# Kernel optimization log

Hardware: AMD Instinct MI355X
Metric: run time of the kernel (lower is better)

Reference implementation:

```python
import jax, jax.numpy as jnp
import numpy as np

HEADS = 4
DIM_HEAD = 32
DIM = 64
NUM_MEM = 4


def _rmsnorm(t, g, dim):
    # F.normalize(x, dim=1) * g * sqrt(dim)  (eps=1e-12 like torch)
    n = jnp.sqrt(jnp.sum(t * t, axis=1, keepdims=True))
    return t / jnp.maximum(n, 1e-12) * g * (dim ** 0.5)


def setup_inputs() -> dict:
    key = jax.random.key(0)
    ks = jax.random.split(key, 7)
    b, c, H, W, D = 2, DIM, 48, 48, 48
    hidden = HEADS * DIM_HEAD
    x = jax.random.normal(ks[0], (b, c, H, W, D), dtype=jnp.float32)
    g_in = jnp.ones((1, c, 1, 1, 1), dtype=jnp.float32)
    w_qkv = jax.random.normal(ks[1], (hidden * 3, c), dtype=jnp.float32) * 0.02  # 1x1 conv3d
    mem_kv = jax.random.normal(ks[2], (2, HEADS, DIM_HEAD, NUM_MEM), dtype=jnp.float32)
    w_out = jax.random.normal(ks[3], (c, hidden), dtype=jnp.float32) * 0.02
    b_out = jnp.zeros((c,), dtype=jnp.float32)
    g_out = jnp.ones((1, c, 1, 1, 1), dtype=jnp.float32)
    return {"x": x, "g_in": g_in, "w_qkv": w_qkv, "mem_kv": mem_kv,
            "w_out": w_out, "b_out": b_out, "g_out": g_out}


def reference(x, g_in, w_qkv, mem_kv, w_out, b_out, g_out):
    b, c, H, W, D = x.shape
    n = H * W * D
    scale = DIM_HEAD ** -0.5
    xn = _rmsnorm(x, g_in, c)
    # 1x1 conv3d == channel matmul
    qkv = jnp.einsum('oc,bcxyz->boxyz', w_qkv, xn)
    q, k, v = jnp.split(qkv, 3, axis=1)
    to_heads = lambda t: t.reshape(b, HEADS, DIM_HEAD, n)
    q, k, v = map(to_heads, (q, k, v))
    mk = jnp.broadcast_to(mem_kv[0], (b, HEADS, DIM_HEAD, NUM_MEM))
    mv = jnp.broadcast_to(mem_kv[1], (b, HEADS, DIM_HEAD, NUM_MEM))
    k = jnp.concatenate([mk, k], axis=-1)
    v = jnp.concatenate([mv, v], axis=-1)
    q = jax.nn.softmax(q, axis=-2) * scale  # softmax over head dim
    k = jax.nn.softmax(k, axis=-1)          # softmax over sequence dim
    context = jnp.einsum('bhdn,bhen->bhde', k, v)   # [b,h,d,e]
    out = jnp.einsum('bhde,bhdn->bhen', context, q)  # [b,h,e,n]
    out = out.reshape(b, HEADS * DIM_HEAD, H, W, D)
    out = jnp.einsum('oc,bcxyz->boxyz', w_out, out) + b_out[None, :, None, None, None]
    return _rmsnorm(out, g_out, c)
```

## Files before the change

### kernel.cpp

```cpp
#include <hip/hip_runtime.h>
#include <math.h>

#define NPOS 110592

typedef float f32x4 __attribute__((ext_vector_type(4)));
typedef short bf16x8 __attribute__((ext_vector_type(8)));
typedef unsigned u32;
typedef u32 u32x2 __attribute__((ext_vector_type(2)));
typedef u32 u32x4 __attribute__((ext_vector_type(4)));

#define MFMA __builtin_amdgcn_mfma_f32_16x16x32_bf16

__device__ __forceinline__ short f2bf(float f) {
    u32 u = __builtin_bit_cast(u32, f);
    u += 0x7fffu + ((u >> 16) & 1u);
    return (short)(u >> 16);
}
__device__ __forceinline__ u32 pack2(float a, float b) {
    return (u32)(unsigned short)f2bf(a) | ((u32)(unsigned short)f2bf(b) << 16);
}

union FragU { u32 w[4]; bf16x8 v; };
__device__ __forceinline__ bf16x8 padfrag(u32 a, u32 b) {
    FragU f; f.w[0] = a; f.w[1] = b; f.w[2] = 0u; f.w[3] = 0u; return f.v;
}

__global__ __launch_bounds__(256) void la_prep(const float* __restrict__ wqkv,
                                               const float* __restrict__ g_in,
                                               short* __restrict__ wqkv_bf)
{
    int i = blockIdx.x * 256 + threadIdx.x;
    if (i < 24576) wqkv_bf[i] = f2bf(wqkv[i] * g_in[i & 63]);
}

__global__ __launch_bounds__(256, 3) void la_p01(
    const float* __restrict__ x, const short* __restrict__ wkv,
    short* __restrict__ xnT, float* __restrict__ partials)
{
    __shared__ __align__(16) char smem[34816];
    char* xnz = smem;
    float (*lctx)[2][32][33] = (float (*)[2][32][33])smem;
    float (*lz)[2][32]       = (float (*)[2][32])(smem + 33792);

    const int tid = threadIdx.x, lane = tid & 63, wid = tid >> 6;
    const int g = lane >> 4, m = lane & 15;
    const int blk = blockIdx.x;
    const int batch = blk / 432;
    const int pb = (blk % 432) * 256;

    const float* base = x + (size_t)batch * 64 * NPOS + pb + tid;
    float xv[64]; float ss = 0.f;
#pragma unroll
    for (int c = 0; c < 64; ++c) { float t = base[(size_t)c * NPOS]; xv[c] = t; ss += t * t; }
    float rn = 8.0f / fmaxf(sqrtf(ss), 1e-12f);

    char* row = xnz + tid * 128;
#pragma unroll
    for (int ch = 0; ch < 8; ++ch) {
        u32x4 w;
        w.x = pack2(xv[ch*8+0] * rn, xv[ch*8+1] * rn);
        w.y = pack2(xv[ch*8+2] * rn, xv[ch*8+3] * rn);
        w.z = pack2(xv[ch*8+4] * rn, xv[ch*8+5] * rn);
        w.w = pack2(xv[ch*8+6] * rn, xv[ch*8+7] * rn);
        *(u32x4*)(row + ((ch ^ (tid & 7)) << 4)) = w;
    }
    __syncthreads();

    const int cg = wid >> 1, hbase = (wid & 1) * 2;

    bf16x8 wkA[2][2][2], wvA[2][2][2];
#pragma unroll
    for (int hh = 0; hh < 2; ++hh) {
#pragma unroll
        for (int dt = 0; dt < 2; ++dt) {
            const short* wr = wkv + (size_t)(128 + (hbase + hh) * 32 + dt * 16 + m) * 64 + g * 8;
            wkA[hh][dt][0] = *(const bf16x8*)wr;
            wkA[hh][dt][1] = *(const bf16x8*)(wr + 32);
        }
#pragma unroll
        for (int et = 0; et < 2; ++et) {
            const short* wr = wkv + (size_t)(256 + (hbase + hh) * 32 + et * 16 + m) * 64 + g * 8;
            wvA[hh][et][0] = *(const bf16x8*)wr;
            wvA[hh][et][1] = *(const bf16x8*)(wr + 32);
        }
    }

    f32x4 acc[2][2][2];
#pragma unroll
    for (int hh = 0; hh < 2; ++hh)
#pragma unroll
        for (int dt = 0; dt < 2; ++dt)
#pragma unroll
            for (int et = 0; et < 2; ++et) acc[hh][dt][et] = (f32x4){0.f, 0.f, 0.f, 0.f};
    float zacc[2][2] = {{0.f, 0.f}, {0.f, 0.f}};

#pragma unroll 1
    for (int ic = 0; ic < 4; ++ic) {
        bf16x8 af[2][2];
#pragma unroll
        for (int mt = 0; mt < 2; ++mt)
#pragma unroll
            for (int kf = 0; kf < 2; ++kf) {
                int rowi = cg * 128 + ic * 32 + mt * 16 + m;
                af[mt][kf] = *(const bf16x8*)(xnz + rowi * 128 + (((kf*4+g) ^ (rowi & 7)) << 4));
            }
#pragma unroll
        for (int hh = 0; hh < 2; ++hh) {
            u32 ek[2][2][2], vv[2][2][2];
#pragma unroll
            for (int dt = 0; dt < 2; ++dt) {
#pragma unroll
                for (int mt = 0; mt < 2; ++mt) {
                    f32x4 a = {0.f, 0.f, 0.f, 0.f};
                    a = MFMA(af[mt][0], wkA[hh][dt][0], a, 0, 0, 0);
                    a = MFMA(af[mt][1], wkA[hh][dt][1], a, 0, 0, 0);
                    float e0 = __expf(a[0]), e1 = __expf(a[1]);
                    float e2 = __expf(a[2]), e3 = __expf(a[3]);
                    zacc[hh][dt] += (e0 + e1) + (e2 + e3);
                    ek[dt][mt][0] = pack2(e0, e1);
                    ek[dt][mt][1] = pack2(e2, e3);
                }
            }
#pragma unroll
            for (int et = 0; et < 2; ++et) {
#pragma unroll
                for (int mt = 0; mt < 2; ++mt) {
                    f32x4 a = {0.f, 0.f, 0.f, 0.f};
                    a = MFMA(af[mt][0], wvA[hh][et][0], a, 0, 0, 0);
                    a = MFMA(af[mt][1], wvA[hh][et][1], a, 0, 0, 0);
                    vv[et][mt][0] = pack2(a[0], a[1]);
                    vv[et][mt][1] = pack2(a[2], a[3]);
                }
            }
#pragma unroll
            for (int dt = 0; dt < 2; ++dt)
#pragma unroll
                for (int et = 0; et < 2; ++et)
#pragma unroll
                    for (int mt = 0; mt < 2; ++mt)
                        acc[hh][dt][et] = MFMA(padfrag(ek[dt][mt][0], ek[dt][mt][1]),
                                               padfrag(vv[et][mt][0], vv[et][mt][1]),
                                               acc[hh][dt][et], 0, 0, 0);
        }
    }

    char* dst = (char*)xnT + ((size_t)batch * NPOS + pb) * 128;
#pragma unroll
    for (int i = 0; i < 8; ++i) {
        int u = i * 256 + tid;
        int r = u >> 3, cl = u & 7;
        u32x4 w = *(const u32x4*)(xnz + r * 128 + ((cl ^ (r & 7)) << 4));
        *(u32x4*)(dst + (size_t)u * 16) = w;
    }

    __syncthreads();
#pragma unroll
    for (int hh = 0; hh < 2; ++hh) {
#pragma unroll
        for (int dt = 0; dt < 2; ++dt) {
#pragma unroll
            for (int et = 0; et < 2; ++et)
#pragma unroll
                for (int r4 = 0; r4 < 4; ++r4)
                    lctx[wid][hh][dt * 16 + g * 4 + r4][et * 16 + m] = acc[hh][dt][et][r4];
            float z = zacc[hh][dt];
            z += __shfl_xor(z, 16);
            z += __shfl_xor(z, 32);
            if (g == 0) lz[wid][hh][dt * 16 + m] = z;
        }
    }
    __syncthreads();

    float* P = partials + (size_t)blk * 4224;
    for (int i = tid; i < 4096; i += 256) {
        int h = i >> 10, de = i & 1023, d = de >> 5, e = de & 31;
        int w0 = h >> 1, hh2 = h & 1;
        P[i] = lctx[w0][hh2][d][e] + lctx[w0 + 2][hh2][d][e];
    }
    if (tid < 128) {
        int h = tid >> 5, d = tid & 31;
        P[4096 + tid] = lz[h >> 1][h & 1][d] + lz[(h >> 1) + 2][h & 1][d];
    }
}

__global__ __launch_bounds__(256) void la_ctxt_a(const float* __restrict__ partials,
                                                 float* __restrict__ part2)
{
    int t = blockIdx.x * 256 + threadIdx.x;
    int b = t / 67584;
    int rem = t % 67584;
    int grp = rem / 4224;
    int i = rem % 4224;
    const float* P = partials + ((size_t)(b * 432 + grp * 27)) * 4224 + i;
    float s = 0.f;
#pragma unroll 3
    for (int j = 0; j < 27; ++j) s += P[(size_t)j * 4224];
    part2[((size_t)(b * 16 + grp)) * 4224 + i] = s;
}

__global__ __launch_bounds__(256) void la_ctxt_b(const float* __restrict__ part2,
                                                 const float* __restrict__ mem_kv,
                                                 const float* __restrict__ wout_f,
                                                 short* __restrict__ W2bf)
{
    __shared__ float ctxN[32][33];
    const int tid = threadIdx.x;
    const int b = blockIdx.x >> 2, h = blockIdx.x & 3;
    const float* P = part2 + (size_t)b * 16 * 4224;
#pragma unroll
    for (int u = 0; u < 4; ++u) {
        int de = tid * 4 + u;
        int d = de >> 5, e = de & 31;
        float S = 0.f, Z = 0.f;
#pragma unroll 4
        for (int grp = 0; grp < 16; ++grp) {
            S += P[(size_t)grp * 4224 + h * 1024 + de];
            Z += P[(size_t)grp * 4224 + 4096 + h * 32 + d];
        }
        const float* mk = mem_kv + (h * 32 + d) * 4;
        const float* mv = mem_kv + 512 + (h * 32 + e) * 4;
#pragma unroll
        for (int mm = 0; mm < 4; ++mm) {
            float ekv = __expf(mk[mm]);
            S += ekv * mv[mm];
            Z += ekv;
        }
        ctxN[d][e] = S / Z;
    }
    __syncthreads();
#pragma unroll
    for (int u = 0; u < 8; ++u) {
        int idx = u * 256 + tid;
        int c = idx >> 5, d = idx & 31;
        const float* wr = wout_f + c * 128 + h * 32;
        float s = 0.f;
#pragma unroll
        for (int e = 0; e < 32; ++e) s += wr[e] * ctxN[d][e];
        W2bf[(size_t)(b * 64 + c) * 128 + h * 32 + d] = f2bf(s);
    }
}

__global__ __launch_bounds__(256, 2) void la_pass2(
    const short* __restrict__ xnT, const short* __restrict__ wq,
    const short* __restrict__ W2, const float* __restrict__ b_out,
    const float* __restrict__ g_out, float* __restrict__ out)
{
    const int tid = threadIdx.x, lane = tid & 63, wid = tid >> 6;
    const int g = lane >> 4, m = lane & 15;
    const int blk = blockIdx.x;
    const int batch = blk / 432;
    const int task = (blk % 432) * 4 + wid;
    const int posbase = task * 64;

    const short* xp = xnT + ((size_t)batch * NPOS + posbase) * 64;
    bf16x8 af[4][2];
#pragma unroll
    for (int mt = 0; mt < 4; ++mt)
#pragma unroll
        for (int kf = 0; kf < 2; ++kf)
            af[mt][kf] = *(const bf16x8*)(xp + (mt * 16 + m) * 64 + kf * 32 + g * 8);

    f32x4 oacc[4][4];
#pragma unroll
    for (int ct = 0; ct < 4; ++ct)
#pragma unroll
        for (int mt = 0; mt < 4; ++mt) oacc[ct][mt] = (f32x4){0.f, 0.f, 0.f, 0.f};

    const float scale = 0.17677669529663687f;
    const short* w2b = W2 + (size_t)batch * 8192;

#pragma unroll 1
    for (int h = 0; h < 4; ++h) {
        f32x4 aa[2][4];
#pragma unroll
        for (int dt = 0; dt < 2; ++dt) {
            const short* wr = wq + (size_t)(h * 32 + dt * 16 + m) * 64 + g * 8;
            bf16x8 a0 = *(const bf16x8*)wr;
            bf16x8 a1 = *(const bf16x8*)(wr + 32);
#pragma unroll
            for (int mt = 0; mt < 4; ++mt) {
                f32x4 a = {0.f, 0.f, 0.f, 0.f};
                a = MFMA(a0, af[mt][0], a, 0, 0, 0);
                a = MFMA(a1, af[mt][1], a, 0, 0, 0);
                aa[dt][mt][0] = __expf(a[0]);
                aa[dt][mt][1] = __expf(a[1]);
                aa[dt][mt][2] = __expf(a[2]);
                aa[dt][mt][3] = __expf(a[3]);
            }
        }
        float inv[4];
#pragma unroll
        for (int mt = 0; mt < 4; ++mt) {
            float dn = (aa[0][mt][0] + aa[0][mt][1]) + (aa[0][mt][2] + aa[0][mt][3])
                     + (aa[1][mt][0] + aa[1][mt][1]) + (aa[1][mt][2] + aa[1][mt][3]);
            dn += __shfl_xor(dn, 16);
            dn += __shfl_xor(dn, 32);
            inv[mt] = scale / dn;
        }
        u32 eqn[2][4][2];
#pragma unroll
        for (int dt = 0; dt < 2; ++dt)
#pragma unroll
            for (int mt = 0; mt < 4; ++mt) {
                eqn[dt][mt][0] = pack2(aa[dt][mt][0] * inv[mt], aa[dt][mt][1] * inv[mt]);
                eqn[dt][mt][1] = pack2(aa[dt][mt][2] * inv[mt], aa[dt][mt][3] * inv[mt]);
            }
#pragma unroll
        for (int ct = 0; ct < 4; ++ct)
#pragma unroll
            for (int dt = 0; dt < 2; ++dt) {
                u32x2 wv = *(const u32x2*)(w2b + (ct * 16 + m) * 128 + h * 32 + dt * 16 + g * 4);
                bf16x8 wfr = padfrag(wv.x, wv.y);
#pragma unroll
                for (int mt = 0; mt < 4; ++mt)
                    oacc[ct][mt] = MFMA(wfr, padfrag(eqn[dt][mt][0], eqn[dt][mt][1]),
                                        oacc[ct][mt], 0, 0, 0);
            }
    }

    float bo[4][4], go[4][4];
#pragma unroll
    for (int ct = 0; ct < 4; ++ct)
#pragma unroll
        for (int r = 0; r < 4; ++r) {
            int c = ct * 16 + g * 4 + r;
            bo[ct][r] = b_out[c];
            go[ct][r] = g_out[c];
        }
    float* ob = out + (size_t)batch * 64 * NPOS;
#pragma unroll
    for (int mt = 0; mt < 4; ++mt) {
        float vv[4][4]; float s2 = 0.f;
#pragma unroll
        for (int ct = 0; ct < 4; ++ct)
#pragma unroll
            for (int r = 0; r < 4; ++r) {
                float v = oacc[ct][mt][r] + bo[ct][r];
                vv[ct][r] = v;
                s2 += v * v;
            }
        s2 += __shfl_xor(s2, 16);
        s2 += __shfl_xor(s2, 32);
        float rn2 = 8.0f / fmaxf(sqrtf(s2), 1e-12f);
        int pn = posbase + mt * 16 + m;
#pragma unroll
        for (int ct = 0; ct < 4; ++ct)
#pragma unroll
            for (int r = 0; r < 4; ++r)
                ob[(size_t)(ct * 16 + g * 4 + r) * NPOS + pn] = vv[ct][r] * rn2 * go[ct][r];
    }
}

extern "C" void kernel_launch(void* const* d_in, const int* in_sizes, int n_in,
                              void* d_out, int out_size, void* d_ws, size_t ws_size,
                              hipStream_t stream) {
    const float* x      = (const float*)d_in[0];
    const float* g_in   = (const float*)d_in[1];
    const float* w_qkv  = (const float*)d_in[2];
    const float* mem_kv = (const float*)d_in[3];
    const float* w_out  = (const float*)d_in[4];
    const float* b_out  = (const float*)d_in[5];
    const float* g_out  = (const float*)d_in[6];
    float* out = (float*)d_out;

    char* ws = (char*)d_ws;
    short* xnT     = (short*)(ws);
    float* part2   = (float*)(ws + 28311552);
    short* wqkv_bf = (short*)(ws + 28852224);
    short* W2bf    = (short*)(ws + 28901376);

    float* partials = (float*)d_out;

    la_prep<<<96, 256, 0, stream>>>(w_qkv, g_in, wqkv_bf);
    la_p01<<<864, 256, 0, stream>>>(x, wqkv_bf, xnT, partials);
    la_ctxt_a<<<528, 256, 0, stream>>>(partials, part2);
    la_ctxt_b<<<8, 256, 0, stream>>>(part2, mem_kv, w_out, W2bf);
    la_pass2<<<864, 256, 0, stream>>>(xnT, wqkv_bf, W2bf, b_out, g_out, out);
}
```

Before: 98.02 us.

## Fuse linear-attention passes into one cooperative persistent kernel with grid syncs

```diff
diff --git a/kernel.cpp b/kernel.cpp
--- a/kernel.cpp
+++ b/kernel.cpp
@@ -1,5 +1,8 @@
 #include <hip/hip_runtime.h>
+#include <hip/hip_cooperative_groups.h>
 #include <math.h>
+
+namespace cg = cooperative_groups;
 
 #define NPOS 110592
 
@@ -31,6 +34,297 @@
 {
     int i = blockIdx.x * 256 + threadIdx.x;
     if (i < 24576) wqkv_bf[i] = f2bf(wqkv[i] * g_in[i & 63]);
+}
+
+__global__ __launch_bounds__(256, 4) void la_fused(
+    const float* __restrict__ x, const short* __restrict__ wqkv,
+    const float* __restrict__ mem_kv, const float* __restrict__ wout_f,
+    const float* __restrict__ b_out, const float* __restrict__ g_out,
+    float* __restrict__ partials, float* __restrict__ ctxG,
+    short* __restrict__ W2bf, float* __restrict__ out)
+{
+    __shared__ __align__(16) char xnz[32768];
+    __shared__ float lctx[32][33];
+    __shared__ float lz[32];
+
+    const int tid = threadIdx.x, lane = tid & 63, wid = tid >> 6;
+    const int g = lane >> 4, m = lane & 15;
+    const int blk = blockIdx.x;
+    const int batch = blk / 432;
+    const int pb = (blk % 432) * 256;
+
+    {
+        const float* base = x + (size_t)batch * 64 * NPOS + pb + tid;
+        float xv[64]; float ss = 0.f;
+#pragma unroll
+        for (int c = 0; c < 64; ++c) { float t = base[(size_t)c * NPOS]; xv[c] = t; ss += t * t; }
+        float rn = 8.0f / fmaxf(sqrtf(ss), 1e-12f);
+        char* row = xnz + tid * 128;
+#pragma unroll
+        for (int ch = 0; ch < 8; ++ch) {
+            u32x4 w;
+            w.x = pack2(xv[ch*8+0] * rn, xv[ch*8+1] * rn);
+            w.y = pack2(xv[ch*8+2] * rn, xv[ch*8+3] * rn);
+            w.z = pack2(xv[ch*8+4] * rn, xv[ch*8+5] * rn);
+            w.w = pack2(xv[ch*8+6] * rn, xv[ch*8+7] * rn);
+            *(u32x4*)(row + ((ch ^ (tid & 7)) << 4)) = w;
+        }
+    }
+    __syncthreads();
+
+    const int cgrp = wid >> 1, hbase = (wid & 1) * 2;
+    f32x4 acc[2][2][2];
+#pragma unroll
+    for (int hh = 0; hh < 2; ++hh)
+#pragma unroll
+        for (int dt = 0; dt < 2; ++dt)
+#pragma unroll
+            for (int et = 0; et < 2; ++et) acc[hh][dt][et] = (f32x4){0.f, 0.f, 0.f, 0.f};
+    float zacc[2][2] = {{0.f, 0.f}, {0.f, 0.f}};
+
+#pragma unroll 1
+    for (int ic = 0; ic < 4; ++ic) {
+        bf16x8 af[2][2];
+#pragma unroll
+        for (int mt = 0; mt < 2; ++mt)
+#pragma unroll
+            for (int kf = 0; kf < 2; ++kf) {
+                int rowi = cgrp * 128 + ic * 32 + mt * 16 + m;
+                af[mt][kf] = *(const bf16x8*)(xnz + rowi * 128 + (((kf*4+g) ^ (rowi & 7)) << 4));
+            }
+#pragma unroll
+        for (int hh = 0; hh < 2; ++hh) {
+            const int h = hbase + hh;
+            u32 ek[2][2][2], vv[2][2][2];
+#pragma unroll
+            for (int dt = 0; dt < 2; ++dt) {
+                const short* wr = wqkv + (size_t)(128 + h * 32 + dt * 16 + m) * 64 + g * 8;
+                bf16x8 w0 = *(const bf16x8*)wr;
+                bf16x8 w1 = *(const bf16x8*)(wr + 32);
+#pragma unroll
+                for (int mt = 0; mt < 2; ++mt) {
+                    f32x4 a = {0.f, 0.f, 0.f, 0.f};
+                    a = MFMA(af[mt][0], w0, a, 0, 0, 0);
+                    a = MFMA(af[mt][1], w1, a, 0, 0, 0);
+                    float e0 = __expf(a[0]), e1 = __expf(a[1]);
+                    float e2 = __expf(a[2]), e3 = __expf(a[3]);
+                    zacc[hh][dt] += (e0 + e1) + (e2 + e3);
+                    ek[dt][mt][0] = pack2(e0, e1);
+                    ek[dt][mt][1] = pack2(e2, e3);
+                }
+            }
+#pragma unroll
+            for (int et = 0; et < 2; ++et) {
+                const short* wr = wqkv + (size_t)(256 + h * 32 + et * 16 + m) * 64 + g * 8;
+                bf16x8 w0 = *(const bf16x8*)wr;
+                bf16x8 w1 = *(const bf16x8*)(wr + 32);
+#pragma unroll
+                for (int mt = 0; mt < 2; ++mt) {
+                    f32x4 a = {0.f, 0.f, 0.f, 0.f};
+                    a = MFMA(af[mt][0], w0, a, 0, 0, 0);
+                    a = MFMA(af[mt][1], w1, a, 0, 0, 0);
+                    vv[et][mt][0] = pack2(a[0], a[1]);
+                    vv[et][mt][1] = pack2(a[2], a[3]);
+                }
+            }
+#pragma unroll
+            for (int dt = 0; dt < 2; ++dt)
+#pragma unroll
+                for (int et = 0; et < 2; ++et)
+#pragma unroll
+                    for (int mt = 0; mt < 2; ++mt)
+                        acc[hh][dt][et] = MFMA(padfrag(ek[dt][mt][0], ek[dt][mt][1]),
+                                               padfrag(vv[et][mt][0], vv[et][mt][1]),
+                                               acc[hh][dt][et], 0, 0, 0);
+        }
+    }
+
+    float ctxsum[4][4];
+#pragma unroll
+    for (int H = 0; H < 4; ++H)
+#pragma unroll
+        for (int k = 0; k < 4; ++k) ctxsum[H][k] = 0.f;
+    float zsum = 0.f;
+
+#pragma unroll
+    for (int r = 0; r < 8; ++r) {
+        const int w = r >> 1, hh = r & 1;
+        const int H = (w & 1) * 2 + hh;
+        if (wid == w) {
+#pragma unroll
+            for (int dt = 0; dt < 2; ++dt) {
+#pragma unroll
+                for (int et = 0; et < 2; ++et)
+#pragma unroll
+                    for (int r4 = 0; r4 < 4; ++r4)
+                        lctx[dt * 16 + g * 4 + r4][et * 16 + m] = acc[hh][dt][et][r4];
+                float z = zacc[hh][dt];
+                z += __shfl_xor(z, 16);
+                z += __shfl_xor(z, 32);
+                if (g == 0) lz[dt * 16 + m] = z;
+            }
+        }
+        __syncthreads();
+#pragma unroll
+        for (int k = 0; k < 4; ++k) {
+            int cell = tid * 4 + k;
+            ctxsum[H][k] += lctx[cell >> 5][cell & 31];
+        }
+        if ((tid >> 5) == H) zsum += lz[tid & 31];
+        __syncthreads();
+    }
+    {
+        float* P = partials + (size_t)blk * 4224;
+#pragma unroll
+        for (int H = 0; H < 4; ++H) {
+            f32x4 v;
+            v[0] = ctxsum[H][0]; v[1] = ctxsum[H][1];
+            v[2] = ctxsum[H][2]; v[3] = ctxsum[H][3];
+            *(f32x4*)(P + H * 1024 + tid * 4) = v;
+        }
+        if (tid < 128) P[4096 + tid] = zsum;
+    }
+
+    cg::this_grid().sync();
+
+    if (blk < 132) {
+        int t = blk * 256 + tid;
+        int q = t / 8448;
+        int u = t % 8448;
+        int b = u / 4224, i = u % 4224;
+        const float* Q = partials + ((size_t)(b * 432 + q * 108)) * 4224 + i;
+        float s = 0.f;
+#pragma unroll 8
+        for (int j = 0; j < 108; ++j) s += Q[(size_t)j * 4224];
+        atomicAdd(&ctxG[b * 4224 + i], s);
+    }
+    cg::this_grid().sync();
+
+    if (blk < 8) {
+        float (*ctxN)[33] = lctx;
+        const int b = blk >> 2, h = blk & 3;
+#pragma unroll
+        for (int u = 0; u < 4; ++u) {
+            int de = tid * 4 + u;
+            int d = de >> 5, e = de & 31;
+            float S = ctxG[b * 4224 + h * 1024 + de];
+            float Z = ctxG[b * 4224 + 4096 + h * 32 + d];
+            const float* mk = mem_kv + (h * 32 + d) * 4;
+            const float* mv = mem_kv + 512 + (h * 32 + e) * 4;
+#pragma unroll
+            for (int mm = 0; mm < 4; ++mm) {
+                float ekv = __expf(mk[mm]);
+                S += ekv * mv[mm];
+                Z += ekv;
+            }
+            ctxN[d][e] = S / Z;
+        }
+        __syncthreads();
+#pragma unroll
+        for (int u = 0; u < 8; ++u) {
+            int idx = u * 256 + tid;
+            int c = idx >> 5, d = idx & 31;
+            const float* wr = wout_f + c * 128 + h * 32;
+            float s = 0.f;
+#pragma unroll
+            for (int e = 0; e < 32; ++e) s += wr[e] * ctxN[d][e];
+            W2bf[(size_t)(b * 64 + c) * 128 + h * 32 + d] = f2bf(s);
+        }
+    }
+    cg::this_grid().sync();
+
+    const short* w2b = W2bf + (size_t)batch * 8192;
+    const float scale = 0.17677669529663687f;
+    float* ob = out + (size_t)batch * 64 * NPOS;
+
+#pragma unroll 1
+    for (int half = 0; half < 2; ++half) {
+        bf16x8 af[2][2];
+#pragma unroll
+        for (int mt = 0; mt < 2; ++mt)
+#pragma unroll
+            for (int kf = 0; kf < 2; ++kf) {
+                int rowi = wid * 64 + half * 32 + mt * 16 + m;
+                af[mt][kf] = *(const bf16x8*)(xnz + rowi * 128 + (((kf*4+g) ^ (rowi & 7)) << 4));
+            }
+        f32x4 oacc[4][2];
+#pragma unroll
+        for (int ct = 0; ct < 4; ++ct)
+#pragma unroll
+            for (int mt = 0; mt < 2; ++mt) oacc[ct][mt] = (f32x4){0.f, 0.f, 0.f, 0.f};
+
+#pragma unroll 1
+        for (int h = 0; h < 4; ++h) {
+            f32x4 aa[2][2];
+#pragma unroll
+            for (int dt = 0; dt < 2; ++dt) {
+                const short* wr = wqkv + (size_t)(h * 32 + dt * 16 + m) * 64 + g * 8;
+                bf16x8 a0 = *(const bf16x8*)wr;
+                bf16x8 a1 = *(const bf16x8*)(wr + 32);
+#pragma unroll
+                for (int mt = 0; mt < 2; ++mt) {
+                    f32x4 a = {0.f, 0.f, 0.f, 0.f};
+                    a = MFMA(a0, af[mt][0], a, 0, 0, 0);
+                    a = MFMA(a1, af[mt][1], a, 0, 0, 0);
+                    aa[dt][mt][0] = __expf(a[0]);
+                    aa[dt][mt][1] = __expf(a[1]);
+                    aa[dt][mt][2] = __expf(a[2]);
+                    aa[dt][mt][3] = __expf(a[3]);
+                }
+            }
+            float inv[2];
+#pragma unroll
+            for (int mt = 0; mt < 2; ++mt) {
+                float dn = (aa[0][mt][0] + aa[0][mt][1]) + (aa[0][mt][2] + aa[0][mt][3])
+                         + (aa[1][mt][0] + aa[1][mt][1]) + (aa[1][mt][2] + aa[1][mt][3]);
+                dn += __shfl_xor(dn, 16);
+                dn += __shfl_xor(dn, 32);
+                inv[mt] = scale / dn;
+            }
+            u32 eqn[2][2][2];
+#pragma unroll
+            for (int dt = 0; dt < 2; ++dt)
+#pragma unroll
+                for (int mt = 0; mt < 2; ++mt) {
+                    eqn[dt][mt][0] = pack2(aa[dt][mt][0] * inv[mt], aa[dt][mt][1] * inv[mt]);
+                    eqn[dt][mt][1] = pack2(aa[dt][mt][2] * inv[mt], aa[dt][mt][3] * inv[mt]);
+                }
+#pragma unroll
+            for (int ct = 0; ct < 4; ++ct)
+#pragma unroll
+                for (int dt = 0; dt < 2; ++dt) {
+                    u32x2 wv = *(const u32x2*)(w2b + (ct * 16 + m) * 128 + h * 32 + dt * 16 + g * 4);
+                    bf16x8 wfr = padfrag(wv.x, wv.y);
+#pragma unroll
+                    for (int mt = 0; mt < 2; ++mt)
+                        oacc[ct][mt] = MFMA(wfr, padfrag(eqn[dt][mt][0], eqn[dt][mt][1]),
+                                            oacc[ct][mt], 0, 0, 0);
+                }
+        }
+
+#pragma unroll
+        for (int mt = 0; mt < 2; ++mt) {
+            float vv[4][4]; float s2 = 0.f;
+#pragma unroll
+            for (int ct = 0; ct < 4; ++ct)
+#pragma unroll
+                for (int r = 0; r < 4; ++r) {
+                    float v = oacc[ct][mt][r] + b_out[ct * 16 + g * 4 + r];
+                    vv[ct][r] = v;
+                    s2 += v * v;
+                }
+            s2 += __shfl_xor(s2, 16);
+            s2 += __shfl_xor(s2, 32);
+            float rn2 = 8.0f / fmaxf(sqrtf(s2), 1e-12f);
+            int pn = pb + wid * 64 + half * 32 + mt * 16 + m;
+#pragma unroll
+            for (int ct = 0; ct < 4; ++ct)
+#pragma unroll
+                for (int r = 0; r < 4; ++r)
+                    ob[(size_t)(ct * 16 + g * 4 + r) * NPOS + pn] =
+                        vv[ct][r] * rn2 * g_out[ct * 16 + g * 4 + r];
+        }
+    }
 }
 
 __global__ __launch_bounds__(256, 3) void la_p01(
@@ -53,7 +347,6 @@
 #pragma unroll
     for (int c = 0; c < 64; ++c) { float t = base[(size_t)c * NPOS]; xv[c] = t; ss += t * t; }
     float rn = 8.0f / fmaxf(sqrtf(ss), 1e-12f);
-
     char* row = xnz + tid * 128;
 #pragma unroll
     for (int ch = 0; ch < 8; ++ch) {
@@ -66,8 +359,7 @@
     }
     __syncthreads();
 
-    const int cg = wid >> 1, hbase = (wid & 1) * 2;
-
+    const int cgrp = wid >> 1, hbase = (wid & 1) * 2;
     bf16x8 wkA[2][2][2], wvA[2][2][2];
 #pragma unroll
     for (int hh = 0; hh < 2; ++hh) {
@@ -84,7 +376,6 @@
             wvA[hh][et][1] = *(const bf16x8*)(wr + 32);
         }
     }
-
     f32x4 acc[2][2][2];
 #pragma unroll
     for (int hh = 0; hh < 2; ++hh)
@@ -101,14 +392,14 @@
         for (int mt = 0; mt < 2; ++mt)
 #pragma unroll
             for (int kf = 0; kf < 2; ++kf) {
-                int rowi = cg * 128 + ic * 32 + mt * 16 + m;
+                int rowi = cgrp * 128 + ic * 32 + mt * 16 + m;
                 af[mt][kf] = *(const bf16x8*)(xnz + rowi * 128 + (((kf*4+g) ^ (rowi & 7)) << 4));
             }
 #pragma unroll
         for (int hh = 0; hh < 2; ++hh) {
             u32 ek[2][2][2], vv[2][2][2];
 #pragma unroll
-            for (int dt = 0; dt < 2; ++dt) {
+            for (int dt = 0; dt < 2; ++dt)
 #pragma unroll
                 for (int mt = 0; mt < 2; ++mt) {
                     f32x4 a = {0.f, 0.f, 0.f, 0.f};
@@ -120,9 +411,8 @@
                     ek[dt][mt][0] = pack2(e0, e1);
                     ek[dt][mt][1] = pack2(e2, e3);
                 }
-            }
-#pragma unroll
-            for (int et = 0; et < 2; ++et) {
+#pragma unroll
+            for (int et = 0; et < 2; ++et)
 #pragma unroll
                 for (int mt = 0; mt < 2; ++mt) {
                     f32x4 a = {0.f, 0.f, 0.f, 0.f};
@@ -131,7 +421,6 @@
                     vv[et][mt][0] = pack2(a[0], a[1]);
                     vv[et][mt][1] = pack2(a[2], a[3]);
                 }
-            }
 #pragma unroll
             for (int dt = 0; dt < 2; ++dt)
 #pragma unroll
@@ -155,7 +444,7 @@
 
     __syncthreads();
 #pragma unroll
-    for (int hh = 0; hh < 2; ++hh) {
+    for (int hh = 0; hh < 2; ++hh)
 #pragma unroll
         for (int dt = 0; dt < 2; ++dt) {
 #pragma unroll
@@ -168,7 +457,6 @@
             z += __shfl_xor(z, 32);
             if (g == 0) lz[wid][hh][dt * 16 + m] = z;
         }
-    }
     __syncthreads();
 
     float* P = partials + (size_t)blk * 4224;
@@ -364,16 +652,38 @@
     float* out = (float*)d_out;
 
     char* ws = (char*)d_ws;
-    short* xnT     = (short*)(ws);
-    float* part2   = (float*)(ws + 28311552);
-    short* wqkv_bf = (short*)(ws + 28852224);
-    short* W2bf    = (short*)(ws + 28901376);
-
-    float* partials = (float*)d_out;
-
-    la_prep<<<96, 256, 0, stream>>>(w_qkv, g_in, wqkv_bf);
-    la_p01<<<864, 256, 0, stream>>>(x, wqkv_bf, xnT, partials);
-    la_ctxt_a<<<528, 256, 0, stream>>>(partials, part2);
-    la_ctxt_b<<<8, 256, 0, stream>>>(part2, mem_kv, w_out, W2bf);
-    la_pass2<<<864, 256, 0, stream>>>(xnT, wqkv_bf, W2bf, b_out, g_out, out);
-}
+    float* partials = (float*)ws;
+    float* ctxG     = (float*)(ws + 14598144);
+    short* wqkv_bf  = (short*)(ws + 14631936);
+    short* W2bf     = (short*)(ws + 14681088);
+
+    int nb = 0;
+    hipError_t qe = hipOccupancyMaxActiveBlocksPerMultiprocessor(
+        &nb, reinterpret_cast<const void*>(la_fused), 256, 0);
+    if (qe == hipSuccess && nb >= 4) {
+        la_prep<<<96, 256, 0, stream>>>(w_qkv, g_in, wqkv_bf);
+        hipMemsetAsync(ctxG, 0, 33792, stream);
+        const float* xa = x; const short* wa = wqkv_bf;
+        const float* ma = mem_kv; const float* wo = w_out;
+        const float* ba = b_out; const float* ga = g_out;
+        float* pa = partials; float* ca = ctxG; short* w2a = W2bf; float* oa = out;
+        void* args[] = {(void*)&xa, (void*)&wa, (void*)&ma, (void*)&wo, (void*)&ba,
+                        (void*)&ga, (void*)&pa, (void*)&ca, (void*)&w2a, (void*)&oa};
+        hipError_t e = hipLaunchCooperativeKernel(
+            reinterpret_cast<const void*>(la_fused), dim3(864), dim3(256), args, 0, stream);
+        if (e == hipSuccess) return;
+        (void)hipGetLastError();
+    }
+
+    short* xnT      = (short*)ws;
+    float* part2    = (float*)(ws + 28311552);
+    short* wqkv_bf2 = (short*)(ws + 28852224);
+    short* W2bf2    = (short*)(ws + 28901376);
+    float* partialsF = (float*)d_out;
+
+    la_prep<<<96, 256, 0, stream>>>(w_qkv, g_in, wqkv_bf2);
+    la_p01<<<864, 256, 0, stream>>>(x, wqkv_bf2, xnT, partialsF);
+    la_ctxt_a<<<528, 256, 0, stream>>>(partialsF, part2);
+    la_ctxt_b<<<8, 256, 0, stream>>>(part2, mem_kv, w_out, W2bf2);
+    la_pass2<<<864, 256, 0, stream>>>(xnT, wqkv_bf2, W2bf2, b_out, g_out, out);
+}
```

New measurement: 97.56 us. No clear change (-0.5%).

## Halve la_p01 tile to 128 positions, split channel loads across thread pairs

Applied to the files above, without the earlier changes.

```diff
diff --git a/kernel.cpp b/kernel.cpp
--- a/kernel.cpp
+++ b/kernel.cpp
@@ -33,36 +33,39 @@
     if (i < 24576) wqkv_bf[i] = f2bf(wqkv[i] * g_in[i & 63]);
 }
 
-__global__ __launch_bounds__(256, 3) void la_p01(
+__global__ __launch_bounds__(256, 6) void la_p01(
     const float* __restrict__ x, const short* __restrict__ wkv,
     short* __restrict__ xnT, float* __restrict__ partials)
 {
-    __shared__ __align__(16) char smem[34816];
+    __shared__ __align__(16) char smem[17920];
     char* xnz = smem;
     float (*lctx)[2][32][33] = (float (*)[2][32][33])smem;
-    float (*lz)[2][32]       = (float (*)[2][32])(smem + 33792);
+    float (*lz)[2][32]       = (float (*)[2][32])(smem + 16896);
 
     const int tid = threadIdx.x, lane = tid & 63, wid = tid >> 6;
     const int g = lane >> 4, m = lane & 15;
     const int blk = blockIdx.x;
-    const int batch = blk / 432;
-    const int pb = (blk % 432) * 256;
-
-    const float* base = x + (size_t)batch * 64 * NPOS + pb + tid;
-    float xv[64]; float ss = 0.f;
-#pragma unroll
-    for (int c = 0; c < 64; ++c) { float t = base[(size_t)c * NPOS]; xv[c] = t; ss += t * t; }
-    float rn = 8.0f / fmaxf(sqrtf(ss), 1e-12f);
-
-    char* row = xnz + tid * 128;
-#pragma unroll
-    for (int ch = 0; ch < 8; ++ch) {
-        u32x4 w;
-        w.x = pack2(xv[ch*8+0] * rn, xv[ch*8+1] * rn);
-        w.y = pack2(xv[ch*8+2] * rn, xv[ch*8+3] * rn);
-        w.z = pack2(xv[ch*8+4] * rn, xv[ch*8+5] * rn);
-        w.w = pack2(xv[ch*8+6] * rn, xv[ch*8+7] * rn);
-        *(u32x4*)(row + ((ch ^ (tid & 7)) << 4)) = w;
+    const int batch = blk / 864;
+    const int pb = (blk % 864) * 128;
+
+    {
+        const int p = tid >> 1, chb = (tid & 1) * 32;
+        const float* base = x + ((size_t)batch * 64 + chb) * NPOS + pb + p;
+        float xv[32]; float ss = 0.f;
+#pragma unroll
+        for (int c = 0; c < 32; ++c) { float t = base[(size_t)c * NPOS]; xv[c] = t; ss += t * t; }
+        ss += __shfl_xor(ss, 1);
+        float rn = 8.0f / fmaxf(sqrtf(ss), 1e-12f);
+#pragma unroll
+        for (int q = 0; q < 4; ++q) {
+            u32x4 w;
+            w.x = pack2(xv[q*8+0] * rn, xv[q*8+1] * rn);
+            w.y = pack2(xv[q*8+2] * rn, xv[q*8+3] * rn);
+            w.z = pack2(xv[q*8+4] * rn, xv[q*8+5] * rn);
+            w.w = pack2(xv[q*8+6] * rn, xv[q*8+7] * rn);
+            int ch = (tid & 1) * 4 + q;
+            *(u32x4*)(xnz + p * 128 + ((ch ^ (p & 7)) << 4)) = w;
+        }
     }
     __syncthreads();
 
@@ -95,13 +98,13 @@
     float zacc[2][2] = {{0.f, 0.f}, {0.f, 0.f}};
 
 #pragma unroll 1
-    for (int ic = 0; ic < 4; ++ic) {
+    for (int ic = 0; ic < 2; ++ic) {
         bf16x8 af[2][2];
 #pragma unroll
         for (int mt = 0; mt < 2; ++mt)
 #pragma unroll
             for (int kf = 0; kf < 2; ++kf) {
-                int rowi = cg * 128 + ic * 32 + mt * 16 + m;
+                int rowi = cg * 64 + ic * 32 + mt * 16 + m;
                 af[mt][kf] = *(const bf16x8*)(xnz + rowi * 128 + (((kf*4+g) ^ (rowi & 7)) << 4));
             }
 #pragma unroll
@@ -146,7 +149,7 @@
 
     char* dst = (char*)xnT + ((size_t)batch * NPOS + pb) * 128;
 #pragma unroll
-    for (int i = 0; i < 8; ++i) {
+    for (int i = 0; i < 4; ++i) {
         int u = i * 256 + tid;
         int r = u >> 3, cl = u & 7;
         u32x4 w = *(const u32x4*)(xnz + r * 128 + ((cl ^ (r & 7)) << 4));
@@ -154,32 +157,50 @@
     }
 
     __syncthreads();
-#pragma unroll
-    for (int hh = 0; hh < 2; ++hh) {
-#pragma unroll
-        for (int dt = 0; dt < 2; ++dt) {
-#pragma unroll
-            for (int et = 0; et < 2; ++et)
-#pragma unroll
-                for (int r4 = 0; r4 < 4; ++r4)
-                    lctx[wid][hh][dt * 16 + g * 4 + r4][et * 16 + m] = acc[hh][dt][et][r4];
-            float z = zacc[hh][dt];
-            z += __shfl_xor(z, 16);
-            z += __shfl_xor(z, 32);
-            if (g == 0) lz[wid][hh][dt * 16 + m] = z;
-        }
+    const int hp = wid & 1;
+    if (wid < 2) {
+#pragma unroll
+        for (int hh = 0; hh < 2; ++hh)
+#pragma unroll
+            for (int dt = 0; dt < 2; ++dt) {
+#pragma unroll
+                for (int et = 0; et < 2; ++et)
+#pragma unroll
+                    for (int r4 = 0; r4 < 4; ++r4)
+                        lctx[hp][hh][dt * 16 + g * 4 + r4][et * 16 + m] = acc[hh][dt][et][r4];
+                float z = zacc[hh][dt];
+                z += __shfl_xor(z, 16);
+                z += __shfl_xor(z, 32);
+                if (g == 0) lz[hp][hh][dt * 16 + m] = z;
+            }
+    }
+    __syncthreads();
+    if (wid >= 2) {
+#pragma unroll
+        for (int hh = 0; hh < 2; ++hh)
+#pragma unroll
+            for (int dt = 0; dt < 2; ++dt) {
+#pragma unroll
+                for (int et = 0; et < 2; ++et)
+#pragma unroll
+                    for (int r4 = 0; r4 < 4; ++r4)
+                        lctx[hp][hh][dt * 16 + g * 4 + r4][et * 16 + m] += acc[hh][dt][et][r4];
+                float z = zacc[hh][dt];
+                z += __shfl_xor(z, 16);
+                z += __shfl_xor(z, 32);
+                if (g == 0) lz[hp][hh][dt * 16 + m] += z;
+            }
     }
     __syncthreads();
 
     float* P = partials + (size_t)blk * 4224;
     for (int i = tid; i < 4096; i += 256) {
         int h = i >> 10, de = i & 1023, d = de >> 5, e = de & 31;
-        int w0 = h >> 1, hh2 = h & 1;
-        P[i] = lctx[w0][hh2][d][e] + lctx[w0 + 2][hh2][d][e];
+        P[i] = lctx[h >> 1][h & 1][d][e];
     }
     if (tid < 128) {
         int h = tid >> 5, d = tid & 31;
-        P[4096 + tid] = lz[h >> 1][h & 1][d] + lz[(h >> 1) + 2][h & 1][d];
+        P[4096 + tid] = lz[h >> 1][h & 1][d];
     }
 }
 
@@ -191,10 +212,10 @@
     int rem = t % 67584;
     int grp = rem / 4224;
     int i = rem % 4224;
-    const float* P = partials + ((size_t)(b * 432 + grp * 27)) * 4224 + i;
+    const float* P = partials + ((size_t)(b * 864 + grp * 54)) * 4224 + i;
     float s = 0.f;
-#pragma unroll 3
-    for (int j = 0; j < 27; ++j) s += P[(size_t)j * 4224];
+#pragma unroll 6
+    for (int j = 0; j < 54; ++j) s += P[(size_t)j * 4224];
     part2[((size_t)(b * 16 + grp)) * 4224 + i] = s;
 }
 
@@ -372,7 +393,7 @@
     float* partials = (float*)d_out;
 
     la_prep<<<96, 256, 0, stream>>>(w_qkv, g_in, wqkv_bf);
-    la_p01<<<864, 256, 0, stream>>>(x, wqkv_bf, xnT, partials);
+    la_p01<<<1728, 256, 0, stream>>>(x, wqkv_bf, xnT, partials);
     la_ctxt_a<<<528, 256, 0, stream>>>(partials, part2);
     la_ctxt_b<<<8, 256, 0, stream>>>(part2, mem_kv, w_out, W2bf);
     la_pass2<<<864, 256, 0, stream>>>(xnT, wqkv_bf, W2bf, b_out, g_out, out);
```

After: 185.3 us. 1.89x slower.
